# Performance work log

Measured on AMD Instinct MI355X. Metric: run time of the kernel, lower is better.

Reference implementation:

```python
import jax, jax.numpy as jnp
import numpy as np

IMG, P, C = 512, 16, 1
D, DEPTH, H, DH, MLP = 768, 12, 8, 64, 2048
GRID = IMG // P          # 32
NP = GRID * GRID         # 1024 patches
N = NP + 1               # +cls token
EPS = 1e-5


def _ln(x, s, b):
    m = jnp.mean(x, -1, keepdims=True)
    v = jnp.mean((x - m) ** 2, -1, keepdims=True)
    return (x - m) * jax.lax.rsqrt(v + EPS) * s + b


def setup_inputs() -> dict:
    key = jax.random.key(0)
    ks = jax.random.split(key, 12)
    s = 0.02
    f32 = jnp.float32
    return {
        "x": jax.random.normal(ks[0], (4, C, IMG, IMG), f32),
        "conv_w": jax.random.normal(ks[1], (D, C, P, P), f32) * s,   # [out,in,kh,kw] like torch
        "conv_b": jnp.zeros((D,), f32),
        "cls_token": jax.random.normal(ks[2], (1, 1, D), f32),
        "pos_emb": jax.random.normal(ks[3], (1, N, D), f32),
        "qkv_w": jax.random.normal(ks[4], (DEPTH, D, 3 * H * DH), f32) * s,  # [in,out] layout
        "merge_w": jax.random.normal(ks[5], (DEPTH, H * DH, D), f32) * s,
        "merge_b": jnp.zeros((DEPTH, D), f32),
        "ln1_s": jnp.ones((DEPTH, D), f32),
        "ln1_b": jnp.zeros((DEPTH, D), f32),
        "ln2_s": jnp.ones((DEPTH, D), f32),
        "ln2_b": jnp.zeros((DEPTH, D), f32),
        "ffn_w1": jax.random.normal(ks[6], (DEPTH, D, MLP), f32) * s,
        "ffn_b1": jnp.zeros((DEPTH, MLP), f32),
        "ffn_w2": jax.random.normal(ks[7], (DEPTH, MLP, D), f32) * s,
        "ffn_b2": jnp.zeros((DEPTH, D), f32),
        "lnf_s": jnp.ones((D,), f32),
        "lnf_b": jnp.zeros((D,), f32),
    }


def reference(x, conv_w, conv_b, cls_token, pos_emb, qkv_w, merge_w, merge_b,
              ln1_s, ln1_b, ln2_s, ln2_b, ffn_w1, ffn_b1, ffn_w2, ffn_b2,
              lnf_s, lnf_b):
    B = x.shape[0]
    # Patch embed: stride-P conv == non-overlapping patch extraction + matmul
    xr = x.reshape(B, C, GRID, P, GRID, P)
    tok = jnp.einsum('bchpwq,dcpq->bhwd', xr, conv_w).reshape(B, NP, D) + conv_b
    t = jnp.concatenate([jnp.broadcast_to(cls_token, (B, 1, D)), tok], axis=1)
    t = t + pos_emb  # dropout is identity in eval
    scale = DH ** -0.5
    for i in range(DEPTH):
        # MSA with pre-LN
        h = _ln(t, ln1_s[i], ln1_b[i])
        qkv = (h @ qkv_w[i]).reshape(B, N, H, 3, DH)   # [B,N,H,3,DH]
        q = jnp.transpose(qkv[..., 0, :], (0, 2, 1, 3))  # [B,H,N,DH]
        k = jnp.transpose(qkv[..., 1, :], (0, 2, 1, 3))
        v = jnp.transpose(qkv[..., 2, :], (0, 2, 1, 3))
        att = jax.nn.softmax(jnp.einsum('bhnd,bhmd->bhnm', q, k) * scale, axis=-1)
        o = jnp.einsum('bhnm,bhmd->bhnd', att, v)
        o = jnp.transpose(o, (0, 2, 1, 3)).reshape(B, N, H * DH)
        t = t + (o @ merge_w[i] + merge_b[i])
        # FFN with pre-LN, exact (erf) GELU like torch nn.GELU
        h2 = _ln(t, ln2_s[i], ln2_b[i])
        f = jax.nn.gelu(h2 @ ffn_w1[i] + ffn_b1[i], approximate=False)
        t = t + (f @ ffn_w2[i] + ffn_b2[i])
    return _ln(t, lnf_s, lnf_b)
```

## Files before the change

kernel.cpp:

```cpp
#include <hip/hip_runtime.h>

#define DEV __device__ __forceinline__

typedef short s8v __attribute__((ext_vector_type(8)));
typedef float f4v __attribute__((ext_vector_type(4)));

DEV short f2bf(float f) {
  unsigned u = __float_as_uint(f);
  u += 0x7FFFu + ((u >> 16) & 1u);
  return (short)(u >> 16);
}
DEV float bf2f(short s) { return __uint_as_float(((unsigned)(unsigned short)s) << 16); }

DEV void gld_lds16(const short* g, short* l) {
  __builtin_amdgcn_global_load_lds(
      (const __attribute__((address_space(1))) void*)g,
      (__attribute__((address_space(3))) void*)l, 16, 0, 0);
}

DEV int xcd_swz(int id, int nwg) {
  int q8 = nwg >> 3, r8 = nwg & 7, xcd = id & 7, off = id >> 3;
  return (xcd < r8) ? (xcd * (q8 + 1) + off) : (r8 * (q8 + 1) + (xcd - r8) * q8 + off);
}

template<int BN>
__global__ __launch_bounds__(256) void gemm_t(
    const short* __restrict__ A, const short* __restrict__ B, void* __restrict__ Cv,
    const float* __restrict__ bias,
    int M, int N, int K, int lda, int ldb, int ldc, int flags)
{
  constexpr int BPASS = BN / 32;
  constexpr int MI = (BN == 128) ? 4 : 2;
  __shared__ __align__(16) short As[2][64 * 64];
  __shared__ __align__(16) short Bs[2][BN * 64];
  int nwg = gridDim.x * gridDim.y;
  int idl = blockIdx.y * gridDim.x + blockIdx.x;
  int swz = xcd_swz(idl, nwg);
  int bx = swz % gridDim.x, by = swz / gridDim.x;
  int m0 = by * 64, n0 = bx * BN;
  int tid = threadIdx.x, lane = tid & 63, w = tid >> 6;
  int lr = lane & 15, kg = lane >> 4;
  int wrb = (BN == 128) ? 0 : (w >> 1) * 32;
  int wcb = (BN == 128) ? w * 32 : (w & 1) * 32;
  f4v acc[MI][2] = {};
  int NT = K >> 6;

#define STAGE(bufi, k0)                                                   \
  {                                                                       \
    _Pragma("unroll")                                                     \
    for (int p = 0; p < 2; ++p) {                                         \
      int ch = p * 256 + w * 64 + lane;                                   \
      int row = ch >> 3, c = (ch & 7) ^ (row & 7);                        \
      gld_lds16(A + (long)(m0 + row) * lda + (k0) + c * 8,                \
                &As[bufi][(p * 256 + w * 64) * 8]);                       \
    }                                                                     \
    _Pragma("unroll")                                                     \
    for (int p = 0; p < BPASS; ++p) {                                     \
      int ch = p * 256 + w * 64 + lane;                                   \
      int row = ch >> 3, c = (ch & 7) ^ (row & 7);                        \
      gld_lds16(B + (long)(n0 + row) * ldb + (k0) + c * 8,                \
                &Bs[bufi][(p * 256 + w * 64) * 8]);                       \
    }                                                                     \
  }

  STAGE(0, 0)
  for (int t = 0; t < NT; ++t) {
    int buf = t & 1;
    if (t + 1 < NT) {
      STAGE(buf ^ 1, (t + 1) * 64)
      if constexpr (BN == 128)
        asm volatile("s_waitcnt vmcnt(6)" ::: "memory");
      else
        asm volatile("s_waitcnt vmcnt(4)" ::: "memory");
    } else {
      asm volatile("s_waitcnt vmcnt(0)" ::: "memory");
    }
    __builtin_amdgcn_s_barrier();
    #pragma unroll
    for (int ks = 0; ks < 2; ++ks) {
      s8v av[MI], bv[2];
      #pragma unroll
      for (int mi = 0; mi < MI; ++mi) {
        int row = wrb + mi * 16 + lr;
        int sl = (ks * 4 + kg) ^ (row & 7);
        av[mi] = *(const s8v*)&As[buf][row * 64 + sl * 8];
      }
      #pragma unroll
      for (int ni = 0; ni < 2; ++ni) {
        int row = wcb + ni * 16 + lr;
        int sl = (ks * 4 + kg) ^ (row & 7);
        bv[ni] = *(const s8v*)&Bs[buf][row * 64 + sl * 8];
      }
      #pragma unroll
      for (int mi = 0; mi < MI; ++mi)
        #pragma unroll
        for (int ni = 0; ni < 2; ++ni)
          acc[mi][ni] = __builtin_amdgcn_mfma_f32_16x16x32_bf16(av[mi], bv[ni], acc[mi][ni], 0, 0, 0);
    }
    asm volatile("s_waitcnt lgkmcnt(0)" ::: "memory");
    __builtin_amdgcn_s_barrier();
  }
#undef STAGE

  float* Cf = (float*)Cv;
  short* Cb = (short*)Cv;
  #pragma unroll
  for (int mi = 0; mi < MI; ++mi)
    #pragma unroll
    for (int ni = 0; ni < 2; ++ni) {
      int col = n0 + wcb + ni * 16 + lr;
      float bvv = (flags & 1) ? bias[col] : 0.f;
      #pragma unroll
      for (int j = 0; j < 4; ++j) {
        int row = m0 + wrb + mi * 16 + kg * 4 + j;
        if (row >= M) continue;
        float v = acc[mi][ni][j] + bvv;
        if (flags & 2) v = 0.5f * v * (1.f + erff(v * 0.70710678118f));
        long ci = (long)row * ldc + col;
        if (flags & 8) Cb[ci] = f2bf(v);
        else { if (flags & 4) v += Cf[ci]; Cf[ci] = v; }
      }
    }
}

__global__ __launch_bounds__(256) void flash_k(
    const short* __restrict__ qkv, float* __restrict__ Opart, float* __restrict__ ML)
{
  int swz = xcd_swz(blockIdx.x, 1088);
  int h = swz / 544, rem = swz - h * 544;
  int z = rem / 17, qt = rem - z * 17;
  int zb = z >> 3, zh = z & 7;
  const short* base = qkv + (long)zb * 1025 * 1536 + zh * 192;
  const short* Qg = base;
  const short* Kg = base + 64;
  const short* Vg = base + 128;
  int q0 = qt * 64;
  int kt0 = h * 9, kt_end = h ? 17 : 9;
  int tid = threadIdx.x, lane = tid & 63, w = tid >> 6;
  int lr = lane & 15, kg = lane >> 4;

  __shared__ __align__(16) short QPs[64][72];
  __shared__ __align__(16) short Ks[2][64 * 64];
  __shared__ __align__(16) short Vt[2][64][72];

  for (int s = tid; s < 512; s += 256) {
    int row = s >> 3, ch = s & 7;
    s8v v = {};
    if (q0 + row < 1025) v = *(const s8v*)(Qg + (long)(q0 + row) * 1536 + ch * 8);
    *(s8v*)&QPs[row][ch * 8] = v;
  }
  __syncthreads();
  s8v aq[2];
  aq[0] = *(const s8v*)&QPs[w * 16 + lr][kg * 8];
  aq[1] = *(const s8v*)&QPs[w * 16 + lr][32 + kg * 8];

#define STAGE_K(bufi, kv0)                                                 \
  {                                                                        \
    int s0 = w * 128;                                                      \
    _Pragma("unroll")                                                      \
    for (int i = 0; i < 2; ++i) {                                          \
      int s = s0 + i * 64 + lane;                                          \
      int row = s >> 3, c = (s & 7) ^ (row & 7);                           \
      gld_lds16(Kg + (long)((kv0) + row) * 1536 + c * 8,                   \
                &Ks[bufi][(s0 + i * 64) * 8]);                             \
    }                                                                      \
  }

  f4v acc[4] = {};
  float m_run[4], l_run[4];
  #pragma unroll
  for (int j = 0; j < 4; ++j) { m_run[j] = -3.0e38f; l_run[j] = 0.f; }

  STAGE_K(0, kt0 * 64)
  #pragma unroll
  for (int p = 0; p < 2; ++p) {
    int s = p * 256 + tid;
    int key = s & 63, ch = s >> 6;
    s8v v = *(const s8v*)(Vg + (long)(kt0 * 64 + key) * 1536 + ch * 8);
    #pragma unroll
    for (int j = 0; j < 8; ++j) Vt[0][ch * 8 + j][key] = v[j];
  }
  asm volatile("s_waitcnt vmcnt(0)" ::: "memory");
  asm volatile("s_waitcnt lgkmcnt(0)" ::: "memory");
  __builtin_amdgcn_s_barrier();

  for (int kt = kt0; kt < kt_end; ++kt) {
    int cur = (kt - kt0) & 1;
    int kv0 = kt * 64;
    s8v vreg[2];
    int vok[2];
    if (kt + 1 < kt_end) {
      STAGE_K(cur ^ 1, kv0 + 64)
      #pragma unroll
      for (int p = 0; p < 2; ++p) {
        int s = p * 256 + tid;
        int key = (s & 63) + kv0 + 64, ch = s >> 6;
        vok[p] = key < 1025;
        vreg[p] = vok[p] ? *(const s8v*)(Vg + (long)key * 1536 + ch * 8) : s8v{};
      }
    }

    f4v sa[4] = {};
    #pragma unroll
    for (int ni = 0; ni < 4; ++ni) {
      int row = ni * 16 + lr;
      #pragma unroll
      for (int ks = 0; ks < 2; ++ks) {
        int c = (ks * 4 + kg) ^ (row & 7);
        s8v bk = *(const s8v*)&Ks[cur][row * 64 + c * 8];
        sa[ni] = __builtin_amdgcn_mfma_f32_16x16x32_bf16(aq[ks], bk, sa[ni], 0, 0, 0);
      }
    }
    float sv[4][4], pv[4][4], tm[4], ts[4];
    #pragma unroll
    for (int j = 0; j < 4; ++j) tm[j] = -3.0e38f;
    #pragma unroll
    for (int ni = 0; ni < 4; ++ni) {
      bool valid = (kv0 + ni * 16 + lr) < 1025;
      #pragma unroll
      for (int j = 0; j < 4; ++j) {
        float s = valid ? sa[ni][j] * 0.125f : -3.0e38f;
        sv[ni][j] = s;
        tm[j] = fmaxf(tm[j], s);
      }
    }
    #pragma unroll
    for (int o = 1; o < 16; o <<= 1)
      #pragma unroll
      for (int j = 0; j < 4; ++j) tm[j] = fmaxf(tm[j], __shfl_xor(tm[j], o));
    float scale[4], m_new[4];
    #pragma unroll
    for (int j = 0; j < 4; ++j) {
      m_new[j] = fmaxf(m_run[j], tm[j]);
      scale[j] = __expf(m_run[j] - m_new[j]);
      m_run[j] = m_new[j];
      ts[j] = 0.f;
    }
    #pragma unroll
    for (int ni = 0; ni < 4; ++ni)
      #pragma unroll
      for (int j = 0; j < 4; ++j) {
        float p = __expf(sv[ni][j] - m_new[j]);
        pv[ni][j] = p;
        ts[j] += p;
      }
    #pragma unroll
    for (int o = 1; o < 16; o <<= 1)
      #pragma unroll
      for (int j = 0; j < 4; ++j) ts[j] += __shfl_xor(ts[j], o);
    #pragma unroll
    for (int j = 0; j < 4; ++j) l_run[j] = l_run[j] * scale[j] + ts[j];
    #pragma unroll
    for (int ni = 0; ni < 4; ++ni)
      #pragma unroll
      for (int j = 0; j < 4; ++j) acc[ni][j] *= scale[j];

    if (kt + 1 < kt_end) {
      #pragma unroll
      for (int p = 0; p < 2; ++p) {
        int s = p * 256 + tid;
        int key = s & 63, ch = s >> 6;
        s8v v = vok[p] ? vreg[p] : s8v{};
        #pragma unroll
        for (int j = 0; j < 8; ++j) Vt[cur ^ 1][ch * 8 + j][key] = v[j];
      }
    }

    #pragma unroll
    for (int ni = 0; ni < 4; ++ni)
      #pragma unroll
      for (int j = 0; j < 4; ++j)
        QPs[w * 16 + kg * 4 + j][ni * 16 + lr] = f2bf(pv[ni][j]);
    asm volatile("s_waitcnt lgkmcnt(0)" ::: "memory");
    s8v ap[2];
    ap[0] = *(const s8v*)&QPs[w * 16 + lr][kg * 8];
    ap[1] = *(const s8v*)&QPs[w * 16 + lr][32 + kg * 8];
    #pragma unroll
    for (int ni = 0; ni < 4; ++ni) {
      #pragma unroll
      for (int ks = 0; ks < 2; ++ks) {
        s8v bvv = *(const s8v*)&Vt[cur][ni * 16 + lr][ks * 32 + kg * 8];
        acc[ni] = __builtin_amdgcn_mfma_f32_16x16x32_bf16(ap[ks], bvv, acc[ni], 0, 0, 0);
      }
    }
    asm volatile("s_waitcnt lgkmcnt(0)" ::: "memory");
    asm volatile("s_waitcnt vmcnt(0)" ::: "memory");
    __builtin_amdgcn_s_barrier();
  }
#undef STAGE_K

  #pragma unroll
  for (int ni = 0; ni < 4; ++ni)
    #pragma unroll
    for (int j = 0; j < 4; ++j) {
      int row = q0 + w * 16 + kg * 4 + j;
      if (row < 1025) {
        long rbase = (long)(h * 32 + z) * 1025 + row;
        Opart[rbase * 64 + ni * 16 + lr] = acc[ni][j];
        if (ni == 0 && lr == 0) {
          ML[rbase * 2]     = m_run[j];
          ML[rbase * 2 + 1] = l_run[j];
        }
      }
    }
}

__global__ __launch_bounds__(256) void fcomb_k(
    const float* __restrict__ Opart, const float* __restrict__ ML, short* __restrict__ O)
{
  int idx = blockIdx.x * 256 + threadIdx.x;
  if (idx >= 32 * 1025 * 64) return;
  int d = idx & 63;
  int r = idx >> 6;
  int z = r / 1025, row = r - z * 1025;
  float m0 = ML[(long)r * 2], l0 = ML[(long)r * 2 + 1];
  float m1 = ML[(long)(32800 + r) * 2], l1 = ML[(long)(32800 + r) * 2 + 1];
  float M = fmaxf(m0, m1);
  float w0 = __expf(m0 - M), w1 = __expf(m1 - M);
  float inv = 1.f / (l0 * w0 + l1 * w1);
  float v = (Opart[(long)r * 64 + d] * w0 + Opart[(long)(32800 + r) * 64 + d] * w1) * inv;
  int zb = z >> 3, zh = z & 7;
  O[((long)(zb * 1025 + row)) * 512 + zh * 64 + d] = f2bf(v);
}

DEV void tconv_body(const float* w, short* wt, int K, int N, int bx, int by, int tid)
{
  __shared__ float tile[32][33];
  int n0 = bx * 32, k0 = by * 32;
  int tx = tid & 31, ty = tid >> 5;
  #pragma unroll
  for (int j = 0; j < 4; ++j)
    tile[ty + j * 8][tx] = w[(long)(k0 + ty + j * 8) * N + n0 + tx];
  __syncthreads();
  #pragma unroll
  for (int j = 0; j < 4; ++j)
    wt[(long)(n0 + ty + j * 8) * K + k0 + tx] = f2bf(tile[tx][ty + j * 8]);
}

__global__ __launch_bounds__(256) void tconv4_k(
    const float* __restrict__ sq, const float* __restrict__ sm,
    const float* __restrict__ sf1, const float* __restrict__ sf2,
    short* __restrict__ dq, short* __restrict__ dm,
    short* __restrict__ df1, short* __restrict__ df2)
{
  int id = blockIdx.x, tid = threadIdx.x;
  if (id < 1152)       tconv_body(sq,  dq,  768, 1536, id % 48,          id / 48,          tid);
  else if (id < 1536)  tconv_body(sm,  dm,  512, 768,  (id - 1152) % 24, (id - 1152) / 24, tid);
  else if (id < 3072)  tconv_body(sf1, df1, 768, 2048, (id - 1536) % 64, (id - 1536) / 64, tid);
  else                 tconv_body(sf2, df2, 2048, 768, (id - 3072) % 24, (id - 3072) / 24, tid);
}

__global__ __launch_bounds__(256) void cvt_k(const float* __restrict__ in,
    short* __restrict__ out, int n)
{
  int i = blockIdx.x * 256 + threadIdx.x;
  if (i < n) out[i] = f2bf(in[i]);
}

DEV void st_ln(float* p, float v) { *p = v; }
DEV void st_ln(short* p, float v) { *p = f2bf(v); }

template<typename OT>
__global__ __launch_bounds__(256) void ln_k(const float* __restrict__ x,
    const float* __restrict__ g, const float* __restrict__ b,
    OT* __restrict__ y, int rows)
{
  int row = blockIdx.x;
  if (row >= rows) return;
  const float* xr = x + (long)row * 768;
  OT* yr = y + (long)row * 768;
  int t = threadIdx.x;
  float v0 = xr[t], v1 = xr[t + 256], v2 = xr[t + 512];
  float s = v0 + v1 + v2, s2 = v0 * v0 + v1 * v1 + v2 * v2;
  #pragma unroll
  for (int o = 32; o > 0; o >>= 1) { s += __shfl_down(s, o); s2 += __shfl_down(s2, o); }
  __shared__ float as_[4], as2_[4];
  if ((t & 63) == 0) { as_[t >> 6] = s; as2_[t >> 6] = s2; }
  __syncthreads();
  s = as_[0] + as_[1] + as_[2] + as_[3];
  s2 = as2_[0] + as2_[1] + as2_[2] + as2_[3];
  float mean = s * (1.f / 768.f);
  float var = s2 * (1.f / 768.f) - mean * mean;
  float r = rsqrtf(var + 1e-5f);
  st_ln(&yr[t],       (v0 - mean) * r * g[t]       + b[t]);
  st_ln(&yr[t + 256], (v1 - mean) * r * g[t + 256] + b[t + 256]);
  st_ln(&yr[t + 512], (v2 - mean) * r * g[t + 512] + b[t + 512]);
}

__global__ __launch_bounds__(256) void im2col_k(const float* __restrict__ x,
    short* __restrict__ A)
{
  int i = blockIdx.x * 256 + threadIdx.x;
  int k = i & 255, row = i >> 8;
  int px = k & 15, py = k >> 4;
  int gx = row & 31, gy = (row >> 5) & 31, b = row >> 10;
  A[i] = f2bf(x[((long)(b * 512) + gy * 16 + py) * 512 + gx * 16 + px]);
}

__global__ __launch_bounds__(256) void assemble_k(const short* __restrict__ tok,
    const float* __restrict__ cls, const float* __restrict__ pos, float* __restrict__ t)
{
  int i = blockIdx.x * 256 + threadIdx.x;
  int d = i % 768; int rn = i / 768; int n = rn % 1025; int b = rn / 1025;
  float v = (n == 0) ? cls[d] : bf2f(tok[((long)(b * 1024 + n - 1)) * 768 + d]);
  t[i] = v + pos[n * 768 + d];
}

extern "C" void kernel_launch(void* const* d_in, const int* in_sizes, int n_in,
                              void* d_out, int out_size, void* d_ws, size_t ws_size,
                              hipStream_t stream)
{
  const float* x       = (const float*)d_in[0];
  const float* conv_w  = (const float*)d_in[1];
  const float* conv_b  = (const float*)d_in[2];
  const float* cls     = (const float*)d_in[3];
  const float* pos     = (const float*)d_in[4];
  const float* qkv_w   = (const float*)d_in[5];
  const float* merge_w = (const float*)d_in[6];
  const float* merge_b = (const float*)d_in[7];
  const float* ln1_s   = (const float*)d_in[8];
  const float* ln1_b   = (const float*)d_in[9];
  const float* ln2_s   = (const float*)d_in[10];
  const float* ln2_b   = (const float*)d_in[11];
  const float* ffn_w1  = (const float*)d_in[12];
  const float* ffn_b1  = (const float*)d_in[13];
  const float* ffn_w2  = (const float*)d_in[14];
  const float* ffn_b2  = (const float*)d_in[15];
  const float* lnf_s   = (const float*)d_in[16];
  const float* lnf_b   = (const float*)d_in[17];

  char* wsp = (char*)d_ws;
  size_t o = 0;
  auto take = [&](size_t bytes) { char* r = wsp + o; o = (o + bytes + 255) & ~(size_t)255; return r; };
  short* wq   = (short*)take(1536ul * 768 * 2);
  short* wm   = (short*)take(768ul * 512 * 2);
  short* wf1  = (short*)take(2048ul * 768 * 2);
  short* wf2  = (short*)take(768ul * 2048 * 2);
  short* wcv  = (short*)take(768ul * 256 * 2);
  float* t    = (float*)take(4100ul * 768 * 4);
  char*  hO   = take(4352ul * 768 * 2);
  short* qkv  = (short*)take(4ul * 1025 * 1536 * 2);
  char*  fV   = take(4352ul * 2048 * 2);
  take(2ul << 20);

  short* h     = (short*)hO;
  short* O     = (short*)hO;
  short* f     = (short*)fV;
  short* imc   = (short*)fV;
  short* tok   = (short*)(fV + 4096ul * 256 * 2);
  float* Opart = (float*)fV;
  float* ML    = (float*)(fV + 16793600);

  dim3 blk(256);

  cvt_k<<<768, blk, 0, stream>>>(conv_w, wcv, 768 * 256);
  im2col_k<<<4096, blk, 0, stream>>>(x, imc);
  gemm_t<64><<<dim3(12, 64), blk, 0, stream>>>(imc, wcv, tok, conv_b,
      4096, 768, 256, 256, 256, 768, 1 | 8);
  assemble_k<<<12300, blk, 0, stream>>>(tok, cls, pos, t);

  for (int i = 0; i < 12; ++i) {
    tconv4_k<<<4608, blk, 0, stream>>>(
        qkv_w + (long)i * 768 * 1536, merge_w + (long)i * 512 * 768,
        ffn_w1 + (long)i * 768 * 2048, ffn_w2 + (long)i * 2048 * 768,
        wq, wm, wf1, wf2);

    ln_k<short><<<4100, blk, 0, stream>>>(t, ln1_s + i * 768, ln1_b + i * 768, h, 4100);
    gemm_t<128><<<dim3(12, 65), blk, 0, stream>>>(h, wq, qkv, nullptr,
        4100, 1536, 768, 768, 768, 1536, 8);
    flash_k<<<1088, blk, 0, stream>>>(qkv, Opart, ML);
    fcomb_k<<<8200, blk, 0, stream>>>(Opart, ML, O);
    gemm_t<64><<<dim3(12, 65), blk, 0, stream>>>(O, wm, t, merge_b + i * 768,
        4100, 768, 512, 512, 512, 768, 1 | 4);
    ln_k<short><<<4100, blk, 0, stream>>>(t, ln2_s + i * 768, ln2_b + i * 768, h, 4100);
    gemm_t<128><<<dim3(16, 65), blk, 0, stream>>>(h, wf1, f, ffn_b1 + i * 2048,
        4100, 2048, 768, 768, 768, 2048, 1 | 2 | 8);
    gemm_t<64><<<dim3(12, 65), blk, 0, stream>>>(f, wf2, t, ffn_b2 + i * 768,
        4100, 768, 2048, 2048, 2048, 768, 1 | 4);
  }
  ln_k<float><<<4100, blk, 0, stream>>>(t, lnf_s, lnf_b, (float*)d_out, 4100);
}
```

Measured before the change: 2.320 ms.

## Drop split-KV flash attention and combine kernel; normalize output in-kernel

The attention kernel no longer splits the key range into two halves. Each block now walks all 17 key tiles and writes the normalized bf16 output directly, so the fp32 partial-output buffers and the separate combine kernel are gone. The softmax now uses exp2 with a log2e-folded scale, applies the key-validity mask only on the last tile, uses a cheaper bf16 rounding for the probabilities, and raises wave priority around the MFMA blocks. The trade-off is half as many blocks (544 instead of 1088) on a large GPU, which lowers occupancy and latency hiding while removing extra memory traffic and one launch per layer.

```diff
diff --git a/kernel.cpp b/kernel.cpp
--- a/kernel.cpp
+++ b/kernel.cpp
@@ -9,6 +9,9 @@
   unsigned u = __float_as_uint(f);
   u += 0x7FFFu + ((u >> 16) & 1u);
   return (short)(u >> 16);
+}
+DEV short f2bf_fast(float f) {
+  return (short)((__float_as_uint(f) + 0x8000u) >> 16);
 }
 DEV float bf2f(short s) { return __uint_as_float(((unsigned)(unsigned short)s) << 16); }
 
@@ -124,18 +127,16 @@
 }
 
 __global__ __launch_bounds__(256) void flash_k(
-    const short* __restrict__ qkv, float* __restrict__ Opart, float* __restrict__ ML)
-{
-  int swz = xcd_swz(blockIdx.x, 1088);
-  int h = swz / 544, rem = swz - h * 544;
-  int z = rem / 17, qt = rem - z * 17;
+    const short* __restrict__ qkv, short* __restrict__ O)
+{
+  int swz = xcd_swz(blockIdx.x, 544);
+  int z = swz / 17, qt = swz - z * 17;
   int zb = z >> 3, zh = z & 7;
   const short* base = qkv + (long)zb * 1025 * 1536 + zh * 192;
   const short* Qg = base;
   const short* Kg = base + 64;
   const short* Vg = base + 128;
   int q0 = qt * 64;
-  int kt0 = h * 9, kt_end = h ? 17 : 9;
   int tid = threadIdx.x, lane = tid & 63, w = tid >> 6;
   int lr = lane & 15, kg = lane >> 4;
 
@@ -170,13 +171,14 @@
   float m_run[4], l_run[4];
   #pragma unroll
   for (int j = 0; j < 4; ++j) { m_run[j] = -3.0e38f; l_run[j] = 0.f; }
-
-  STAGE_K(0, kt0 * 64)
+  const float C2 = 0.18033688011112042f;
+
+  STAGE_K(0, 0)
   #pragma unroll
   for (int p = 0; p < 2; ++p) {
     int s = p * 256 + tid;
     int key = s & 63, ch = s >> 6;
-    s8v v = *(const s8v*)(Vg + (long)(kt0 * 64 + key) * 1536 + ch * 8);
+    s8v v = *(const s8v*)(Vg + (long)key * 1536 + ch * 8);
     #pragma unroll
     for (int j = 0; j < 8; ++j) Vt[0][ch * 8 + j][key] = v[j];
   }
@@ -184,12 +186,12 @@
   asm volatile("s_waitcnt lgkmcnt(0)" ::: "memory");
   __builtin_amdgcn_s_barrier();
 
-  for (int kt = kt0; kt < kt_end; ++kt) {
-    int cur = (kt - kt0) & 1;
+  for (int kt = 0; kt < 17; ++kt) {
+    int cur = kt & 1;
     int kv0 = kt * 64;
     s8v vreg[2];
     int vok[2];
-    if (kt + 1 < kt_end) {
+    if (kt < 16) {
       STAGE_K(cur ^ 1, kv0 + 64)
       #pragma unroll
       for (int p = 0; p < 2; ++p) {
@@ -201,6 +203,7 @@
     }
 
     f4v sa[4] = {};
+    __builtin_amdgcn_s_setprio(1);
     #pragma unroll
     for (int ni = 0; ni < 4; ++ni) {
       int row = ni * 16 + lr;
@@ -211,17 +214,29 @@
         sa[ni] = __builtin_amdgcn_mfma_f32_16x16x32_bf16(aq[ks], bk, sa[ni], 0, 0, 0);
       }
     }
+    __builtin_amdgcn_s_setprio(0);
     float sv[4][4], pv[4][4], tm[4], ts[4];
     #pragma unroll
     for (int j = 0; j < 4; ++j) tm[j] = -3.0e38f;
-    #pragma unroll
-    for (int ni = 0; ni < 4; ++ni) {
-      bool valid = (kv0 + ni * 16 + lr) < 1025;
-      #pragma unroll
-      for (int j = 0; j < 4; ++j) {
-        float s = valid ? sa[ni][j] * 0.125f : -3.0e38f;
-        sv[ni][j] = s;
-        tm[j] = fmaxf(tm[j], s);
+    if (kt != 16) {
+      #pragma unroll
+      for (int ni = 0; ni < 4; ++ni)
+        #pragma unroll
+        for (int j = 0; j < 4; ++j) {
+          float s = sa[ni][j] * C2;
+          sv[ni][j] = s;
+          tm[j] = fmaxf(tm[j], s);
+        }
+    } else {
+      #pragma unroll
+      for (int ni = 0; ni < 4; ++ni) {
+        bool valid = (kv0 + ni * 16 + lr) < 1025;
+        #pragma unroll
+        for (int j = 0; j < 4; ++j) {
+          float s = valid ? sa[ni][j] * C2 : -3.0e38f;
+          sv[ni][j] = s;
+          tm[j] = fmaxf(tm[j], s);
+        }
       }
     }
     #pragma unroll
@@ -232,7 +247,7 @@
     #pragma unroll
     for (int j = 0; j < 4; ++j) {
       m_new[j] = fmaxf(m_run[j], tm[j]);
-      scale[j] = __expf(m_run[j] - m_new[j]);
+      scale[j] = exp2f(m_run[j] - m_new[j]);
       m_run[j] = m_new[j];
       ts[j] = 0.f;
     }
@@ -240,7 +255,7 @@
     for (int ni = 0; ni < 4; ++ni)
       #pragma unroll
       for (int j = 0; j < 4; ++j) {
-        float p = __expf(sv[ni][j] - m_new[j]);
+        float p = exp2f(sv[ni][j] - m_new[j]);
         pv[ni][j] = p;
         ts[j] += p;
       }
@@ -255,7 +270,7 @@
       #pragma unroll
       for (int j = 0; j < 4; ++j) acc[ni][j] *= scale[j];
 
-    if (kt + 1 < kt_end) {
+    if (kt < 16) {
       #pragma unroll
       for (int p = 0; p < 2; ++p) {
         int s = p * 256 + tid;
@@ -270,11 +285,12 @@
     for (int ni = 0; ni < 4; ++ni)
       #pragma unroll
       for (int j = 0; j < 4; ++j)
-        QPs[w * 16 + kg * 4 + j][ni * 16 + lr] = f2bf(pv[ni][j]);
+        QPs[w * 16 + kg * 4 + j][ni * 16 + lr] = f2bf_fast(pv[ni][j]);
     asm volatile("s_waitcnt lgkmcnt(0)" ::: "memory");
     s8v ap[2];
     ap[0] = *(const s8v*)&QPs[w * 16 + lr][kg * 8];
     ap[1] = *(const s8v*)&QPs[w * 16 + lr][32 + kg * 8];
+    __builtin_amdgcn_s_setprio(1);
     #pragma unroll
     for (int ni = 0; ni < 4; ++ni) {
       #pragma unroll
@@ -283,44 +299,24 @@
         acc[ni] = __builtin_amdgcn_mfma_f32_16x16x32_bf16(ap[ks], bvv, acc[ni], 0, 0, 0);
       }
     }
+    __builtin_amdgcn_s_setprio(0);
     asm volatile("s_waitcnt lgkmcnt(0)" ::: "memory");
     asm volatile("s_waitcnt vmcnt(0)" ::: "memory");
     __builtin_amdgcn_s_barrier();
   }
 #undef STAGE_K
 
+  float inv[4];
+  #pragma unroll
+  for (int j = 0; j < 4; ++j) inv[j] = 1.f / l_run[j];
   #pragma unroll
   for (int ni = 0; ni < 4; ++ni)
     #pragma unroll
     for (int j = 0; j < 4; ++j) {
       int row = q0 + w * 16 + kg * 4 + j;
-      if (row < 1025) {
-        long rbase = (long)(h * 32 + z) * 1025 + row;
-        Opart[rbase * 64 + ni * 16 + lr] = acc[ni][j];
-        if (ni == 0 && lr == 0) {
-          ML[rbase * 2]     = m_run[j];
-          ML[rbase * 2 + 1] = l_run[j];
-        }
-      }
-    }
-}
-
-__global__ __launch_bounds__(256) void fcomb_k(
-    const float* __restrict__ Opart, const float* __restrict__ ML, short* __restrict__ O)
-{
-  int idx = blockIdx.x * 256 + threadIdx.x;
-  if (idx >= 32 * 1025 * 64) return;
-  int d = idx & 63;
-  int r = idx >> 6;
-  int z = r / 1025, row = r - z * 1025;
-  float m0 = ML[(long)r * 2], l0 = ML[(long)r * 2 + 1];
-  float m1 = ML[(long)(32800 + r) * 2], l1 = ML[(long)(32800 + r) * 2 + 1];
-  float M = fmaxf(m0, m1);
-  float w0 = __expf(m0 - M), w1 = __expf(m1 - M);
-  float inv = 1.f / (l0 * w0 + l1 * w1);
-  float v = (Opart[(long)r * 64 + d] * w0 + Opart[(long)(32800 + r) * 64 + d] * w1) * inv;
-  int zb = z >> 3, zh = z & 7;
-  O[((long)(zb * 1025 + row)) * 512 + zh * 64 + d] = f2bf(v);
+      if (row < 1025)
+        O[((long)(zb * 1025 + row)) * 512 + zh * 64 + ni * 16 + lr] = f2bf(acc[ni][j] * inv[j]);
+    }
 }
 
 DEV void tconv_body(const float* w, short* wt, int K, int N, int bx, int by, int tid)
@@ -443,13 +439,11 @@
   char*  fV   = take(4352ul * 2048 * 2);
   take(2ul << 20);
 
-  short* h     = (short*)hO;
-  short* O     = (short*)hO;
-  short* f     = (short*)fV;
-  short* imc   = (short*)fV;
-  short* tok   = (short*)(fV + 4096ul * 256 * 2);
-  float* Opart = (float*)fV;
-  float* ML    = (float*)(fV + 16793600);
+  short* h   = (short*)hO;
+  short* O   = (short*)hO;
+  short* f   = (short*)fV;
+  short* imc = (short*)fV;
+  short* tok = (short*)(fV + 4096ul * 256 * 2);
 
   dim3 blk(256);
 
@@ -468,8 +462,7 @@
     ln_k<short><<<4100, blk, 0, stream>>>(t, ln1_s + i * 768, ln1_b + i * 768, h, 4100);
     gemm_t<128><<<dim3(12, 65), blk, 0, stream>>>(h, wq, qkv, nullptr,
         4100, 1536, 768, 768, 768, 1536, 8);
-    flash_k<<<1088, blk, 0, stream>>>(qkv, Opart, ML);
-    fcomb_k<<<8200, blk, 0, stream>>>(Opart, ML, O);
+    flash_k<<<544, blk, 0, stream>>>(qkv, O);
     gemm_t<64><<<dim3(12, 65), blk, 0, stream>>>(O, wm, t, merge_b + i * 768,
         4100, 768, 512, 512, 512, 768, 1 | 4);
     ln_k<short><<<4100, blk, 0, stream>>>(t, ln2_s + i * 768, ln2_b + i * 768, h, 4100);
```

Result: no change. 2.297 ms (-1.0%).
